# Kernel tuning notes

Measured on AMD Instinct MI355X. Metric: run time of the kernel, lower is better.

Reference implementation:

```python
import jax, jax.numpy as jnp
import numpy as np

NB, NA, NC, NH, NW = 64, 5, 20, 38, 38
MAXT = 40
ANCHORS = jnp.array([[1.3221, 1.73145], [3.19275, 4.00944], [5.05587, 8.09892],
                     [9.47112, 4.84053], [11.2364, 10.0071]], dtype=jnp.float32)
OBJECT_SCALE, NOOBJECT_SCALE = 5.0, 1.0
CLASS_SCALE, COORD_SCALE = 1.0, 1.0
THRESH = 0.4


def setup_inputs() -> dict:
    key = jax.random.key(0)
    k1, k2, k3, k4 = jax.random.split(key, 4)
    output = jax.random.normal(k1, (NB, NA * (5 + NC), NH, NW), dtype=jnp.float32)
    cls_id = jax.random.randint(k2, (NB, MAXT), 0, NC).astype(jnp.float32)
    gxy = jax.random.uniform(k3, (NB, MAXT, 2), minval=0.05, maxval=0.95)
    gwh = jax.random.uniform(k4, (NB, MAXT, 2), minval=0.05, maxval=0.5)
    target = jnp.concatenate([cls_id[..., None], gxy, gwh], axis=-1).reshape(NB, MAXT * 5)
    return {"output": output, "target": target}


def iou_cwh(a, b):
    # boxes in (cx, cy, w, h)
    ax1, ax2 = a[..., 0] - a[..., 2] * 0.5, a[..., 0] + a[..., 2] * 0.5
    ay1, ay2 = a[..., 1] - a[..., 3] * 0.5, a[..., 1] + a[..., 3] * 0.5
    bx1, bx2 = b[..., 0] - b[..., 2] * 0.5, b[..., 0] + b[..., 2] * 0.5
    by1, by2 = b[..., 1] - b[..., 3] * 0.5, b[..., 1] + b[..., 3] * 0.5
    iw = jnp.maximum(jnp.minimum(ax2, bx2) - jnp.maximum(ax1, bx1), 0.0)
    ih = jnp.maximum(jnp.minimum(ay2, by2) - jnp.maximum(ay1, by1), 0.0)
    inter = iw * ih
    union = a[..., 2] * a[..., 3] + b[..., 2] * b[..., 3] - inter
    return inter / union


def smooth_l1_sum(p, t):
    d = jnp.abs(p - t)
    return jnp.sum(jnp.where(d < 1.0, 0.5 * d * d, d - 0.5))


def _forward(output, target):
    nB, nA, nC, nH, nW = NB, NA, NC, NH, NW
    out5 = output.reshape(nB, nA, 5 + nC, nH, nW)
    x = jax.nn.sigmoid(out5[:, :, 0])      # [nB,nA,nH,nW]
    y = jax.nn.sigmoid(out5[:, :, 1])
    w = out5[:, :, 2]
    h = out5[:, :, 3]
    conf = jax.nn.sigmoid(out5[:, :, 4])
    cls_logits = jnp.transpose(out5[:, :, 5:], (0, 1, 3, 4, 2))  # [nB,nA,nH,nW,nC]

    # --- decode predicted boxes (detached, mirrors use of .data in torch) ---
    sg = jax.lax.stop_gradient
    grid_x = jnp.arange(nW, dtype=jnp.float32)[None, None, None, :]
    grid_y = jnp.arange(nH, dtype=jnp.float32)[None, None, :, None]
    aw = ANCHORS[:, 0][None, :, None, None]
    ah = ANCHORS[:, 1][None, :, None, None]
    pred = jnp.stack([sg(x) + grid_x, sg(y) + grid_y,
                      jnp.exp(sg(w)) * aw, jnp.exp(sg(h)) * ah], axis=-1)  # [nB,nA,nH,nW,4]

    # --- build_targets (vectorized) ---
    tgt = target.reshape(nB, MAXT, 5)
    gcls = tgt[..., 0]
    gx, gy = tgt[..., 1] * nW, tgt[..., 2] * nH
    gw, gh = tgt[..., 3] * nW, tgt[..., 4] * nH
    # loop breaks at first zero gx: all later targets invalid
    valid = jnp.cumprod((tgt[..., 1] != 0).astype(jnp.float32), axis=1) > 0  # [nB,40]

    gt_boxes = jnp.stack([gx, gy, gw, gh], axis=-1)                 # [nB,40,4]
    pb = pred.reshape(nB, nA * nH * nW, 4)
    ious = iou_cwh(gt_boxes[:, :, None, :], pb[:, None, :, :])      # [nB,40,nAnchors]
    ious = jnp.where(valid[:, :, None], ious, 0.0)
    cur_ious = jnp.max(ious, axis=1)                                # [nB,nAnchors]
    conf_mask = jnp.where(cur_ious > THRESH, 0.0, NOOBJECT_SCALE).reshape(nB, nA, nH, nW)

    # best anchor per GT: IoU of zero-centered (w,h) boxes
    aws, ahs = ANCHORS[:, 0], ANCHORS[:, 1]
    inter = jnp.minimum(gw[..., None], aws) * jnp.minimum(gh[..., None], ahs)
    a_iou = inter / (gw[..., None] * gh[..., None] + aws * ahs - inter)  # [nB,40,nA]
    best_n = jnp.argmax(a_iou, axis=-1)                                  # [nB,40]

    gi = jnp.clip(gx.astype(jnp.int32), 0, nW - 1)
    gj = jnp.clip(gy.astype(jnp.int32), 0, nH - 1)
    bidx = jnp.broadcast_to(jnp.arange(nB)[:, None], (nB, MAXT))
    gi_s = jnp.where(valid, gi, nW)  # out-of-bounds -> dropped scatter
    idx = (bidx, best_n, gj, gi_s)

    pred_sel = pred[bidx, best_n, gj, gi]        # [nB,40,4]
    t_iou = iou_cwh(gt_boxes, pred_sel)          # [nB,40]
    aw_b, ah_b = aws[best_n], ahs[best_n]
    vtx = gx - gi.astype(jnp.float32)
    vty = gy - gj.astype(jnp.float32)
    vtw = jnp.log(gw / aw_b)
    vth = jnp.log(gh / ah_b)

    zeros = jnp.zeros((nB, nA, nH, nW), dtype=jnp.float32)
    coord_mask = zeros.at[idx].set(1.0, mode='drop')
    cls_mask = coord_mask  # identical writes in torch code
    conf_mask = conf_mask.at[idx].set(OBJECT_SCALE, mode='drop')
    tx = zeros.at[idx].set(vtx, mode='drop')
    ty = zeros.at[idx].set(vty, mode='drop')
    tw = zeros.at[idx].set(vtw, mode='drop')
    th = zeros.at[idx].set(vth, mode='drop')
    tconf = zeros.at[idx].set(t_iou, mode='drop')
    tcls = jnp.zeros((nB, nA, nH, nW), dtype=jnp.int32).at[idx].set(gcls.astype(jnp.int32), mode='drop')

    coord_mask = sg(coord_mask); cls_mask = sg(cls_mask)
    conf_mask = sg(conf_mask)
    tx, ty, tw, th, tconf = sg(tx), sg(ty), sg(tw), sg(th), sg(tconf)

    # --- losses ---
    loss_x = COORD_SCALE * smooth_l1_sum(x * coord_mask, tx * coord_mask) / 2.0
    loss_y = COORD_SCALE * smooth_l1_sum(y * coord_mask, ty * coord_mask) / 2.0
    loss_w = COORD_SCALE * smooth_l1_sum(w * coord_mask, tw * coord_mask) / 2.0
    loss_h = COORD_SCALE * smooth_l1_sum(h * coord_mask, th * coord_mask) / 2.0
    cm = jnp.sqrt(conf_mask)
    loss_conf = jnp.sum((conf * cm - tconf * cm) ** 2) / 2.0
    # focal loss (gamma=2, sum) over cls-masked locations
    logp = jax.nn.log_softmax(cls_logits, axis=-1)
    logpt = jnp.take_along_axis(logp, tcls[..., None], axis=-1)[..., 0]
    pt = jnp.exp(logpt)
    fl = -((1.0 - pt) ** 2) * logpt
    loss_cls = CLASS_SCALE * jnp.sum(cls_mask * fl)

    loss_box = loss_x + loss_y + loss_w + loss_h + loss_conf
    loss = loss_box + loss_cls
    return loss, loss_cls, loss_box


def reference(output, target):
    return _forward(output, target)
```

## Files before the change

### kernel.cpp

```cpp
#include <hip/hip_runtime.h>

#define NB 64
#define NA 5
#define NC 20
#define NH 38
#define NW 38
#define MAXT 40
#define CS (NH * NW)
#define CELLS_PER_B (NA * CS)
#define TPB 256
#define CPT 4
#define CHUNK_CELLS (TPB * CPT)
#define CHUNKS 8
#define NBLK (NB * CHUNKS)

__constant__ float c_aw[NA] = {1.3221f, 3.19275f, 5.05587f, 9.47112f, 11.2364f};
__constant__ float c_ah[NA] = {1.73145f, 4.00944f, 8.09892f, 4.84053f, 10.0071f};

__device__ __forceinline__ float sl1(float d) {
    d = fabsf(d);
    return (d < 1.0f) ? 0.5f * d * d : d - 0.5f;
}
__device__ __forceinline__ float sigm(float x) {
    return __builtin_amdgcn_rcpf(1.0f + __expf(-x));
}

__global__ __launch_bounds__(TPB) void region_kernel(
    const float* __restrict__ outp, const float* __restrict__ tgt,
    float2* __restrict__ partials)
{
    __shared__ float4 s_box[MAXT];
    __shared__ alignas(16) float s_ga[MAXT];
    __shared__ int    s_key[MAXT];

    const int b     = blockIdx.x / CHUNKS;
    const int chunk = blockIdx.x - b * CHUNKS;
    const int tid   = threadIdx.x;

    float w_gx = 0.f, w_gy = 0.f, w_gw = 0.f, w_gh = 0.f;
    int   w_bn = 0, w_gi = 0, w_gj = 0, w_cls = 0, mykey = -1;
    bool  w_valid = false;

    if (tid < 64) {
        const bool is_t = tid < MAXT;
        const float* tb = tgt + b * (MAXT * 5) + tid * 5;
        float t0 = 0.f, t1 = 0.f, t2 = 0.f, t3 = 0.f, t4 = 0.f;
        if (is_t) { t0 = tb[0]; t1 = tb[1]; t2 = tb[2]; t3 = tb[3]; t4 = tb[4]; }
        const unsigned long long nz = __ballot(is_t && (t1 != 0.0f));
        const bool valid = is_t && ((~nz & (((1ull << tid) << 1) - 1ull)) == 0ull);
        if (is_t) {
            float4 mybox = make_float4(3e30f, 3e30f, -3e30f, -3e30f);
            float  myga  = 0.0f;
            if (valid) {
                const float gx = t1 * NW, gy = t2 * NH, gw = t3 * NW, gh = t4 * NH;
                int bn = 0; float best = -1.0f;
                #pragma unroll
                for (int a = 0; a < NA; ++a) {
                    const float inter = fminf(gw, c_aw[a]) * fminf(gh, c_ah[a]);
                    const float aiou  = inter / (gw * gh + c_aw[a] * c_ah[a] - inter);
                    if (aiou > best) { best = aiou; bn = a; }
                }
                const int gi = min(max((int)gx, 0), NW - 1);
                const int gj = min(max((int)gy, 0), NH - 1);
                mybox = make_float4(gx - 0.5f * gw, gy - 0.5f * gh,
                                    gx + 0.5f * gw, gy + 0.5f * gh);
                myga  = 0.4f * gw * gh;
                mykey = bn * CS + gj * NW + gi;
                w_gx = gx; w_gy = gy; w_gw = gw; w_gh = gh;
                w_bn = bn; w_gi = gi; w_gj = gj; w_cls = (int)t0; w_valid = true;
            }
            s_box[tid] = mybox; s_ga[tid] = myga; s_key[tid] = valid ? mykey : -1;
        }
    }
    __syncthreads();

    float box_sum = 0.0f, cls_sum = 0.0f;

    if (chunk == CHUNKS - 1 && w_valid) {
        bool last = true;
        for (int tp = tid + 1; tp < MAXT; ++tp) last &= (s_key[tp] != mykey);
        if (last) {
            const float* cell = outp + (size_t)((b * NA + w_bn) * (5 + NC)) * CS
                                + (w_gj * NW + w_gi);
            const float xo = cell[0],      yo = cell[CS];
            const float wo = cell[2 * CS], ho = cell[3 * CS], co = cell[4 * CS];
            float cls_v[NC];
            #pragma unroll
            for (int q = 0; q < NC; ++q) cls_v[q] = cell[(5 + q) * CS];

            const float sx = sigm(xo), sy = sigm(yo), sc = sigm(co);
            const float pxc = sx + (float)w_gi, pyc = sy + (float)w_gj;
            const float pw = __expf(wo) * c_aw[w_bn], ph = __expf(ho) * c_ah[w_bn];
            const float px1 = pxc - 0.5f * pw, px2 = pxc + 0.5f * pw;
            const float py1 = pyc - 0.5f * ph, py2 = pyc + 0.5f * ph;
            const float pa = pw * ph, p04 = 0.4f * pa;

            bool flag = false;
            for (int t = 0; t < MAXT; ++t) {
                const float4 bx = s_box[t];
                const float iw = fminf(px2, bx.z) - fmaxf(px1, bx.x);
                const float ih = fminf(py2, bx.w) - fmaxf(py1, bx.y);
                const float inter = fmaxf(iw, 0.0f) * fmaxf(ih, 0.0f);
                flag = flag | (1.4f * inter > p04 + s_ga[t]);
            }
            const float cmd = flag ? 0.0f : 1.0f;

            const float gx1 = w_gx - 0.5f * w_gw, gx2 = w_gx + 0.5f * w_gw;
            const float gy1 = w_gy - 0.5f * w_gh, gy2 = w_gy + 0.5f * w_gh;
            const float iw = fminf(px2, gx2) - fmaxf(px1, gx1);
            const float ih = fminf(py2, gy2) - fmaxf(py1, gy1);
            const float inter = fmaxf(iw, 0.f) * fmaxf(ih, 0.f);
            const float tconf = inter / (w_gw * w_gh + pa - inter);

            const float dc = sc - tconf;
            box_sum += 2.5f * dc * dc - 0.5f * cmd * sc * sc;

            const float vtx = w_gx - (float)w_gi, vty = w_gy - (float)w_gj;
            const float vtw = __logf(w_gw / c_aw[w_bn]);
            const float vth = __logf(w_gh / c_ah[w_bn]);
            box_sum += 0.5f * (sl1(sx - vtx) + sl1(sy - vty) +
                               sl1(wo - vtw) + sl1(ho - vth));

            float m = -1e30f;
            #pragma unroll
            for (int q = 0; q < NC; ++q) m = fmaxf(m, cls_v[q]);
            float se = 0.f, lt = 0.f;
            #pragma unroll
            for (int q = 0; q < NC; ++q) {
                se += __expf(cls_v[q] - m);
                if (q == w_cls) lt = cls_v[q];
            }
            const float logpt = lt - (m + __logf(se));
            const float pt = __expf(logpt);
            const float om = 1.0f - pt;
            cls_sum += -(om * om) * logpt;
        }
    }

    {
        const int cbase = chunk * CHUNK_CELLS + tid;
        float px1[CPT], px2[CPT], py1[CPT], py2[CPT], p04[CPT], scv[CPT];
        bool  flag[CPT];

        #pragma unroll
        for (int u = 0; u < CPT; ++u) {
            const int c = cbase + u * TPB;
            flag[u] = false;
            if (c < CELLS_PER_B) {
                const int a = c / CS, r = c - a * CS;
                const int j = r / NW,  i = r - j * NW;
                const float* cell = outp + (size_t)((b * NA + a) * (5 + NC)) * CS + r;
                const float xo = cell[0],      yo = cell[CS];
                const float wo = cell[2 * CS], ho = cell[3 * CS], co = cell[4 * CS];
                const float sx = sigm(xo), sy = sigm(yo);
                scv[u] = sigm(co);
                const float pxc = sx + (float)i, pyc = sy + (float)j;
                const float pw = __expf(wo) * c_aw[a], ph = __expf(ho) * c_ah[a];
                px1[u] = pxc - 0.5f * pw; px2[u] = pxc + 0.5f * pw;
                py1[u] = pyc - 0.5f * ph; py2[u] = pyc + 0.5f * ph;
                p04[u] = 0.4f * (pw * ph);
            } else {
                px1[u] = 3e30f; px2[u] = -3e30f;
                py1[u] = 3e30f; py2[u] = -3e30f;
                p04[u] = 0.0f;  scv[u] = 0.0f;
            }
        }

        #pragma unroll 2
        for (int t4 = 0; t4 < MAXT; t4 += 4) {
            const float4 ga4 = *reinterpret_cast<const float4*>(&s_ga[t4]);
            #pragma unroll
            for (int k = 0; k < 4; ++k) {
                const float4 bx = s_box[t4 + k];
                const float  ga = (k == 0) ? ga4.x : (k == 1) ? ga4.y
                                 : (k == 2) ? ga4.z : ga4.w;
                #pragma unroll
                for (int u = 0; u < CPT; ++u) {
                    const float iw = fminf(px2[u], bx.z) - fmaxf(px1[u], bx.x);
                    const float ih = fminf(py2[u], bx.w) - fmaxf(py1[u], bx.y);
                    const float inter = fmaxf(iw, 0.0f) * fmaxf(ih, 0.0f);
                    flag[u] = flag[u] | (1.4f * inter > p04[u] + ga);
                }
            }
        }

        #pragma unroll
        for (int u = 0; u < CPT; ++u) {
            const float cm = flag[u] ? 0.0f : 1.0f;
            box_sum += 0.5f * cm * scv[u] * scv[u];
        }
    }

    #pragma unroll
    for (int off = 32; off > 0; off >>= 1) {
        box_sum += __shfl_down(box_sum, off);
        cls_sum += __shfl_down(cls_sum, off);
    }
    __shared__ float red[8];
    const int wv = tid >> 6, ln = tid & 63;
    if (ln == 0) { red[wv] = box_sum; red[4 + wv] = cls_sum; }
    __syncthreads();
    if (tid == 0) {
        partials[blockIdx.x] = make_float2(red[0] + red[1] + red[2] + red[3],
                                           red[4] + red[5] + red[6] + red[7]);
    }
}

__global__ __launch_bounds__(256) void finalize_kernel(
    const float2* __restrict__ partials, float* __restrict__ o)
{
    const int tid = threadIdx.x;
    const float2 pa = partials[tid];
    const float2 pb = partials[tid + 256];
    float box = pa.x + pb.x;
    float cls = pa.y + pb.y;
    #pragma unroll
    for (int off = 32; off > 0; off >>= 1) {
        box += __shfl_down(box, off);
        cls += __shfl_down(cls, off);
    }
    __shared__ float red[8];
    const int wv = tid >> 6, ln = tid & 63;
    if (ln == 0) { red[wv] = box; red[4 + wv] = cls; }
    __syncthreads();
    if (tid == 0) {
        const float boxT = red[0] + red[1] + red[2] + red[3];
        const float clsT = red[4] + red[5] + red[6] + red[7];
        o[0] = boxT + clsT;
        o[1] = clsT;
        o[2] = boxT;
    }
}

extern "C" void kernel_launch(void* const* d_in, const int* in_sizes, int n_in,
                              void* d_out, int out_size, void* d_ws, size_t ws_size,
                              hipStream_t stream)
{
    const float* outp = (const float*)d_in[0];
    const float* tgt  = (const float*)d_in[1];
    float2* partials  = (float2*)d_ws;

    region_kernel<<<dim3(NBLK), dim3(TPB), 0, stream>>>(outp, tgt, partials);
    finalize_kernel<<<1, 256, 0, stream>>>(partials, (float*)d_out);
}
```

Before: 21.53 us.

## Split grid into more chunks and hoist cell loads ahead of target setup

```diff
diff --git a/kernel.cpp b/kernel.cpp
--- a/kernel.cpp
+++ b/kernel.cpp
@@ -9,10 +9,11 @@
 #define CS (NH * NW)
 #define CELLS_PER_B (NA * CS)
 #define TPB 256
-#define CPT 4
+#define CPT 2
 #define CHUNK_CELLS (TPB * CPT)
-#define CHUNKS 8
+#define CHUNKS 16
 #define NBLK (NB * CHUNKS)
+#define IOUC (0.4f / 1.4f)
 
 __constant__ float c_aw[NA] = {1.3221f, 3.19275f, 5.05587f, 9.47112f, 11.2364f};
 __constant__ float c_ah[NA] = {1.73145f, 4.00944f, 8.09892f, 4.84053f, 10.0071f};
@@ -33,9 +34,24 @@
     __shared__ alignas(16) float s_ga[MAXT];
     __shared__ int    s_key[MAXT];
 
-    const int b     = blockIdx.x / CHUNKS;
-    const int chunk = blockIdx.x - b * CHUNKS;
+    const int b     = blockIdx.x >> 4;
+    const int chunk = blockIdx.x & 15;
     const int tid   = threadIdx.x;
+
+    const int cbase = chunk * CHUNK_CELLS + tid;
+    float xo[CPT], yo[CPT], wo[CPT], ho[CPT], co[CPT];
+    bool live[CPT];
+    #pragma unroll
+    for (int u = 0; u < CPT; ++u) {
+        const int c  = cbase + u * TPB;
+        live[u] = (c < CELLS_PER_B);
+        const int cc = live[u] ? c : (CELLS_PER_B - 1);
+        const int a  = cc / CS, r = cc - a * CS;
+        const float* cell = outp + (size_t)((b * NA + a) * (5 + NC)) * CS + r;
+        xo[u] = cell[0];      yo[u] = cell[CS];
+        wo[u] = cell[2 * CS]; ho[u] = cell[3 * CS];
+        co[u] = cell[4 * CS];
+    }
 
     float w_gx = 0.f, w_gy = 0.f, w_gw = 0.f, w_gh = 0.f;
     int   w_bn = 0, w_gi = 0, w_gj = 0, w_cls = 0, mykey = -1;
@@ -64,7 +80,7 @@
                 const int gj = min(max((int)gy, 0), NH - 1);
                 mybox = make_float4(gx - 0.5f * gw, gy - 0.5f * gh,
                                     gx + 0.5f * gw, gy + 0.5f * gh);
-                myga  = 0.4f * gw * gh;
+                myga  = IOUC * (gw * gh);
                 mykey = bn * CS + gj * NW + gi;
                 w_gx = gx; w_gy = gy; w_gw = gw; w_gh = gh;
                 w_bn = bn; w_gi = gi; w_gj = gj; w_cls = (int)t0; w_valid = true;
@@ -72,6 +88,23 @@
             s_box[tid] = mybox; s_ga[tid] = myga; s_key[tid] = valid ? mykey : -1;
         }
     }
+
+    float px1[CPT], px2[CPT], py1[CPT], py2[CPT], p04[CPT], scv[CPT];
+    #pragma unroll
+    for (int u = 0; u < CPT; ++u) {
+        const int c = cbase + u * TPB;
+        const int cc = live[u] ? c : 0;
+        const int a = cc / CS, r = cc - a * CS;
+        const int j = r / NW,  i = r - j * NW;
+        const float sx = sigm(xo[u]), sy = sigm(yo[u]);
+        scv[u] = live[u] ? sigm(co[u]) : 0.0f;
+        const float pxc = sx + (float)i, pyc = sy + (float)j;
+        const float pw = __expf(wo[u]) * c_aw[a], ph = __expf(ho[u]) * c_ah[a];
+        px1[u] = pxc - 0.5f * pw; px2[u] = pxc + 0.5f * pw;
+        py1[u] = pyc - 0.5f * ph; py2[u] = pyc + 0.5f * ph;
+        p04[u] = IOUC * (pw * ph);
+    }
+
     __syncthreads();
 
     float box_sum = 0.0f, cls_sum = 0.0f;
@@ -82,33 +115,33 @@
         if (last) {
             const float* cell = outp + (size_t)((b * NA + w_bn) * (5 + NC)) * CS
                                 + (w_gj * NW + w_gi);
-            const float xo = cell[0],      yo = cell[CS];
-            const float wo = cell[2 * CS], ho = cell[3 * CS], co = cell[4 * CS];
+            const float xw = cell[0],      yw = cell[CS];
+            const float ww = cell[2 * CS], hw = cell[3 * CS], cw = cell[4 * CS];
             float cls_v[NC];
             #pragma unroll
             for (int q = 0; q < NC; ++q) cls_v[q] = cell[(5 + q) * CS];
 
-            const float sx = sigm(xo), sy = sigm(yo), sc = sigm(co);
+            const float sx = sigm(xw), sy = sigm(yw), sc = sigm(cw);
             const float pxc = sx + (float)w_gi, pyc = sy + (float)w_gj;
-            const float pw = __expf(wo) * c_aw[w_bn], ph = __expf(ho) * c_ah[w_bn];
-            const float px1 = pxc - 0.5f * pw, px2 = pxc + 0.5f * pw;
-            const float py1 = pyc - 0.5f * ph, py2 = pyc + 0.5f * ph;
-            const float pa = pw * ph, p04 = 0.4f * pa;
+            const float pw = __expf(ww) * c_aw[w_bn], ph = __expf(hw) * c_ah[w_bn];
+            const float wx1 = pxc - 0.5f * pw, wx2 = pxc + 0.5f * pw;
+            const float wy1 = pyc - 0.5f * ph, wy2 = pyc + 0.5f * ph;
+            const float pa = pw * ph, wp04 = IOUC * (pw * ph);
 
             bool flag = false;
             for (int t = 0; t < MAXT; ++t) {
                 const float4 bx = s_box[t];
-                const float iw = fminf(px2, bx.z) - fmaxf(px1, bx.x);
-                const float ih = fminf(py2, bx.w) - fmaxf(py1, bx.y);
+                const float iw = fminf(wx2, bx.z) - fmaxf(wx1, bx.x);
+                const float ih = fminf(wy2, bx.w) - fmaxf(wy1, bx.y);
                 const float inter = fmaxf(iw, 0.0f) * fmaxf(ih, 0.0f);
-                flag = flag | (1.4f * inter > p04 + s_ga[t]);
+                flag = flag | (inter > wp04 + s_ga[t]);
             }
             const float cmd = flag ? 0.0f : 1.0f;
 
             const float gx1 = w_gx - 0.5f * w_gw, gx2 = w_gx + 0.5f * w_gw;
             const float gy1 = w_gy - 0.5f * w_gh, gy2 = w_gy + 0.5f * w_gh;
-            const float iw = fminf(px2, gx2) - fmaxf(px1, gx1);
-            const float ih = fminf(py2, gy2) - fmaxf(py1, gy1);
+            const float iw = fminf(wx2, gx2) - fmaxf(wx1, gx1);
+            const float ih = fminf(wy2, gy2) - fmaxf(wy1, gy1);
             const float inter = fmaxf(iw, 0.f) * fmaxf(ih, 0.f);
             const float tconf = inter / (w_gw * w_gh + pa - inter);
 
@@ -119,7 +152,7 @@
             const float vtw = __logf(w_gw / c_aw[w_bn]);
             const float vth = __logf(w_gh / c_ah[w_bn]);
             box_sum += 0.5f * (sl1(sx - vtx) + sl1(sy - vty) +
-                               sl1(wo - vtw) + sl1(ho - vth));
+                               sl1(ww - vtw) + sl1(hw - vth));
 
             float m = -1e30f;
             #pragma unroll
@@ -135,36 +168,10 @@
             const float om = 1.0f - pt;
             cls_sum += -(om * om) * logpt;
         }
-    }
-
-    {
-        const int cbase = chunk * CHUNK_CELLS + tid;
-        float px1[CPT], px2[CPT], py1[CPT], py2[CPT], p04[CPT], scv[CPT];
-        bool  flag[CPT];
-
+    } else if (chunk != CHUNKS - 1) {
+        bool flag[CPT];
         #pragma unroll
-        for (int u = 0; u < CPT; ++u) {
-            const int c = cbase + u * TPB;
-            flag[u] = false;
-            if (c < CELLS_PER_B) {
-                const int a = c / CS, r = c - a * CS;
-                const int j = r / NW,  i = r - j * NW;
-                const float* cell = outp + (size_t)((b * NA + a) * (5 + NC)) * CS + r;
-                const float xo = cell[0],      yo = cell[CS];
-                const float wo = cell[2 * CS], ho = cell[3 * CS], co = cell[4 * CS];
-                const float sx = sigm(xo), sy = sigm(yo);
-                scv[u] = sigm(co);
-                const float pxc = sx + (float)i, pyc = sy + (float)j;
-                const float pw = __expf(wo) * c_aw[a], ph = __expf(ho) * c_ah[a];
-                px1[u] = pxc - 0.5f * pw; px2[u] = pxc + 0.5f * pw;
-                py1[u] = pyc - 0.5f * ph; py2[u] = pyc + 0.5f * ph;
-                p04[u] = 0.4f * (pw * ph);
-            } else {
-                px1[u] = 3e30f; px2[u] = -3e30f;
-                py1[u] = 3e30f; py2[u] = -3e30f;
-                p04[u] = 0.0f;  scv[u] = 0.0f;
-            }
-        }
+        for (int u = 0; u < CPT; ++u) flag[u] = false;
 
         #pragma unroll 2
         for (int t4 = 0; t4 < MAXT; t4 += 4) {
@@ -179,15 +186,14 @@
                     const float iw = fminf(px2[u], bx.z) - fmaxf(px1[u], bx.x);
                     const float ih = fminf(py2[u], bx.w) - fmaxf(py1[u], bx.y);
                     const float inter = fmaxf(iw, 0.0f) * fmaxf(ih, 0.0f);
-                    flag[u] = flag[u] | (1.4f * inter > p04[u] + ga);
+                    flag[u] = flag[u] | (inter > p04[u] + ga);
                 }
             }
         }
 
         #pragma unroll
         for (int u = 0; u < CPT; ++u) {
-            const float cm = flag[u] ? 0.0f : 1.0f;
-            box_sum += 0.5f * cm * scv[u] * scv[u];
+            if (!flag[u]) box_sum += 0.5f * scv[u] * scv[u];
         }
     }
 
@@ -210,10 +216,12 @@
     const float2* __restrict__ partials, float* __restrict__ o)
 {
     const int tid = threadIdx.x;
-    const float2 pa = partials[tid];
-    const float2 pb = partials[tid + 256];
-    float box = pa.x + pb.x;
-    float cls = pa.y + pb.y;
+    float box = 0.0f, cls = 0.0f;
+    #pragma unroll
+    for (int k = 0; k < 4; ++k) {
+        const float2 p = partials[tid + k * 256];
+        box += p.x; cls += p.y;
+    }
     #pragma unroll
     for (int off = 32; off > 0; off >>= 1) {
         box += __shfl_down(box, off);
```

Result: faster. 18.05 us (-16.2%).
